# Performance work log

Hardware: AMD Instinct MI355X
Metric: run time of the kernel (lower is better)

## Reference

```python
import jax, jax.numpy as jnp
import numpy as np

N = 50000
E = 400000
IN_DIM = 128
HID = 128
OUT = 128
HEADS = 4
NEG_SLOPE = 0.2
EPS = 1e-16


def setup_inputs() -> dict:
    key = jax.random.key(0)
    ks = jax.random.split(key, 12)
    s = 0.05
    return {
        "x": jax.random.normal(ks[0], (N, IN_DIM), dtype=jnp.float32),
        "edge_index": jax.random.randint(ks[1], (2, E), 0, N, dtype=jnp.int64),
        # layer 1: in_dim -> hid, heads=4, concat
        "W1": jax.random.normal(ks[2], (IN_DIM, HEADS * HID), dtype=jnp.float32) * s,
        "att_src1": jax.random.normal(ks[3], (HEADS, HID), dtype=jnp.float32) * s,
        "att_dst1": jax.random.normal(ks[4], (HEADS, HID), dtype=jnp.float32) * s,
        "bias1": jnp.zeros((HEADS * HID,), dtype=jnp.float32),
        # layer 2: hid*heads -> out, heads=1, no concat
        "W2": jax.random.normal(ks[5], (HEADS * HID, OUT), dtype=jnp.float32) * s,
        "att_src2": jax.random.normal(ks[6], (1, OUT), dtype=jnp.float32) * s,
        "att_dst2": jax.random.normal(ks[7], (1, OUT), dtype=jnp.float32) * s,
        "bias2": jnp.zeros((OUT,), dtype=jnp.float32),
    }


def gat_conv(x, src, dst, W, att_src, att_dst, bias, heads, out_dim, concat):
    n = x.shape[0]
    h = (x @ W).reshape(n, heads, out_dim)                       # [N,H,D]
    a_src = jnp.sum(h * att_src[None], axis=-1)                  # [N,H]
    a_dst = jnp.sum(h * att_dst[None], axis=-1)                  # [N,H]
    e = jax.nn.leaky_relu(a_src[src] + a_dst[dst], NEG_SLOPE)    # [E,H]
    # segment softmax over incoming edges of each dst node
    e_max = jax.ops.segment_max(e, dst, num_segments=n)          # [N,H]
    ex = jnp.exp(e - e_max[dst])
    denom = jax.ops.segment_sum(ex, dst, num_segments=n)         # [N,H]
    alpha = ex / (denom[dst] + EPS)                              # [E,H]
    msg = h[src] * alpha[..., None]                              # [E,H,D]
    out = jax.ops.segment_sum(msg, dst, num_segments=n)          # [N,H,D]
    out = out.reshape(n, heads * out_dim) if concat else out.mean(axis=1)
    return out + bias


def reference(x, edge_index, W1, att_src1, att_dst1, bias1, W2, att_src2, att_dst2, bias2):
    n = x.shape[0]
    loop = jnp.arange(n, dtype=edge_index.dtype)
    src = jnp.concatenate([edge_index[0], loop])  # PyG add_self_loops=True
    dst = jnp.concatenate([edge_index[1], loop])
    h = jax.nn.elu(gat_conv(x, src, dst, W1, att_src1, att_dst1, bias1, HEADS, HID, True))
    z = jax.nn.elu(gat_conv(h, src, dst, W2, att_src2, att_dst2, bias2, 1, OUT, False))
    # F.normalize(z, dim=-1): L2 with eps=1e-12 clamp on the norm
    norm = jnp.maximum(jnp.linalg.norm(z, axis=-1, keepdims=True), 1e-12)
    return z / norm
```

## Files before the change

### kernel.cpp

```cpp
#include <hip/hip_runtime.h>
#include <cstddef>

#define N_NODES 50000
#define N_EDGES 400000
#define TOT_EDGES (N_EDGES + N_NODES)
#define M_PAD 50048
#define SCAN_PAD 50176

typedef _Float16 f16;
typedef __attribute__((ext_vector_type(8))) _Float16 f16x8;
typedef __attribute__((ext_vector_type(4))) _Float16 f16x4;
typedef __attribute__((ext_vector_type(2))) _Float16 f16x2;
typedef __attribute__((ext_vector_type(4))) float f32x4;

__global__ void zero_int(int* __restrict__ p, int n) {
  int i = blockIdx.x * blockDim.x + threadIdx.x;
  if (i < n) p[i] = 0;
}

__global__ void count_kernel(const int* __restrict__ ei, int* __restrict__ cnt) {
  int e = blockIdx.x * blockDim.x + threadIdx.x;
  if (e >= TOT_EDGES) return;
  int dst = (e < N_EDGES) ? ei[N_EDGES + e] : (e - N_EDGES);
  atomicAdd(&cnt[dst], 1);
}

__global__ __launch_bounds__(256) void block_scan(const int* __restrict__ cnt,
                                                  int* __restrict__ pre,
                                                  int* __restrict__ bsum) {
  __shared__ int wsum[4];
  const int t = threadIdx.x, lane = t & 63, w = t >> 6;
  const int base = blockIdx.x * 1024 + t * 4;
  int4 v = *(const int4*)&cnt[base];
  const int s = v.x + v.y + v.z + v.w;
  int x = s;
#pragma unroll
  for (int off = 1; off < 64; off <<= 1) {
    int y = __shfl_up(x, off);
    if (lane >= off) x += y;
  }
  if (lane == 63) wsum[w] = x;
  __syncthreads();
  int woff = 0;
  for (int j = 0; j < w; ++j) woff += wsum[j];
  const int ex = x - s + woff;
  pre[base + 0] = ex;
  pre[base + 1] = ex + v.x;
  pre[base + 2] = ex + v.x + v.y;
  pre[base + 3] = ex + v.x + v.y + v.z;
  if (t == 255) bsum[blockIdx.x] = ex + s;
}

__global__ void bsum_scan(int* __restrict__ bsum, int nb) {
  const int lane = threadIdx.x;
  int v = (lane < nb) ? bsum[lane] : 0;
  int x = v;
#pragma unroll
  for (int off = 1; off < 64; off <<= 1) {
    int y = __shfl_up(x, off);
    if (lane >= off) x += y;
  }
  if (lane < nb) bsum[lane] = x - v;
}

__global__ __launch_bounds__(256) void add_off(int* __restrict__ pre,
                                               const int* __restrict__ boff,
                                               int* __restrict__ cursor) {
  const int base = blockIdx.x * 1024 + threadIdx.x * 4;
  const int off = boff[blockIdx.x];
  int4 v = *(const int4*)&pre[base];
  v.x += off; v.y += off; v.z += off; v.w += off;
  *(int4*)&pre[base] = v;
  *(int4*)&cursor[base] = v;
}

__global__ void fill_kernel(const int* __restrict__ ei, int* __restrict__ cursor,
                            int* __restrict__ csr_src) {
  int e = blockIdx.x * blockDim.x + threadIdx.x;
  if (e >= TOT_EDGES) return;
  int s, d;
  if (e < N_EDGES) { s = ei[e]; d = ei[N_EDGES + e]; }
  else             { s = d = e - N_EDGES; }
  int pos = atomicAdd(&cursor[d], 1);
  csr_src[pos] = s;
}

__global__ __launch_bounds__(256) void prep_x(const float* __restrict__ x,
                                              f16* __restrict__ xb,
                                              const float* __restrict__ V1s,
                                              const float* __restrict__ V1d,
                                              float* __restrict__ as1,
                                              float* __restrict__ ad1) {
  const int wid = (blockIdx.x * 256 + threadIdx.x) >> 6;
  const int lane = threadIdx.x & 63;
  if (wid >= M_PAD) return;
  const int k = lane * 2;
  if (wid >= N_NODES) {
    f16x2 z; z[0] = (f16)0.f; z[1] = (f16)0.f;
    *(f16x2*)&xb[(size_t)wid * 128 + k] = z;
    return;
  }
  float2 xv = *(const float2*)&x[(size_t)wid * 128 + k];
  f16x2 o; o[0] = (f16)xv.x; o[1] = (f16)xv.y;
  *(f16x2*)&xb[(size_t)wid * 128 + k] = o;

  float4 vs0 = *(const float4*)&V1s[k * 4];
  float4 vs1 = *(const float4*)&V1s[(k + 1) * 4];
  float4 vd0 = *(const float4*)&V1d[k * 4];
  float4 vd1 = *(const float4*)&V1d[(k + 1) * 4];
  float s[4], d[4];
  s[0] = xv.x * vs0.x + xv.y * vs1.x;
  s[1] = xv.x * vs0.y + xv.y * vs1.y;
  s[2] = xv.x * vs0.z + xv.y * vs1.z;
  s[3] = xv.x * vs0.w + xv.y * vs1.w;
  d[0] = xv.x * vd0.x + xv.y * vd1.x;
  d[1] = xv.x * vd0.y + xv.y * vd1.y;
  d[2] = xv.x * vd0.z + xv.y * vd1.z;
  d[3] = xv.x * vd0.w + xv.y * vd1.w;
#pragma unroll
  for (int h = 0; h < 4; ++h) {
#pragma unroll
    for (int off = 32; off; off >>= 1) {
      s[h] += __shfl_xor(s[h], off);
      d[h] += __shfl_xor(d[h], off);
    }
  }
  if (lane == 0) {
    *(float4*)&as1[(size_t)wid * 4] = make_float4(s[0], s[1], s[2], s[3]);
    *(float4*)&ad1[(size_t)wid * 4] = make_float4(d[0], d[1], d[2], d[3]);
  }
}

__global__ __launch_bounds__(256) void prep_weights(
    const float* __restrict__ W1, const float* __restrict__ W2,
    const float* __restrict__ att_s1, const float* __restrict__ att_d1,
    const float* __restrict__ att_s2, const float* __restrict__ att_d2,
    f16* __restrict__ w1t, f16* __restrict__ w2t,
    float* __restrict__ V1s, float* __restrict__ V1d,
    float* __restrict__ V2s, float* __restrict__ V2d) {
  const int b = blockIdx.x;
  if (b < 256) {
    const int idx = b * 256 + threadIdx.x;
    const int cc = idx >> 7, rr = idx & 127;
    w1t[idx] = (f16)W1[(size_t)rr * 512 + cc];
  } else if (b < 512) {
    const int idx = (b - 256) * 256 + threadIdx.x;
    const int cc = idx >> 9, rr = idx & 511;
    w2t[idx] = (f16)W2[(size_t)rr * 128 + cc];
  } else if (b < 640) {
    const int wid = (b - 512) * 4 + (threadIdx.x >> 6);
    const int lane = threadIdx.x & 63;
    const int k = wid >> 2, h = wid & 3;
    const float* wrow = W1 + (size_t)k * 512 + h * 128;
    float2 wv = *(const float2*)&wrow[lane * 2];
    float2 sv = *(const float2*)&att_s1[h * 128 + lane * 2];
    float2 dv = *(const float2*)&att_d1[h * 128 + lane * 2];
    float ps = wv.x * sv.x + wv.y * sv.y;
    float pd = wv.x * dv.x + wv.y * dv.y;
#pragma unroll
    for (int off = 32; off; off >>= 1) {
      ps += __shfl_xor(ps, off);
      pd += __shfl_xor(pd, off);
    }
    if (lane == 0) { V1s[k * 4 + h] = ps; V1d[k * 4 + h] = pd; }
  } else {
    const int wid = (b - 640) * 4 + (threadIdx.x >> 6);
    const int lane = threadIdx.x & 63;
    const float* wrow = W2 + (size_t)wid * 128;
    float2 wv = *(const float2*)&wrow[lane * 2];
    float2 sv = *(const float2*)&att_s2[lane * 2];
    float2 dv = *(const float2*)&att_d2[lane * 2];
    float ps = wv.x * sv.x + wv.y * sv.y;
    float pd = wv.x * dv.x + wv.y * dv.y;
#pragma unroll
    for (int off = 32; off; off >>= 1) {
      ps += __shfl_xor(ps, off);
      pd += __shfl_xor(pd, off);
    }
    if (lane == 0) { V2s[wid] = ps; V2d[wid] = pd; }
  }
}

template <int K, bool PER_HEAD>
__global__ __launch_bounds__(256) void gemm_bt(const f16* __restrict__ A, int lda,
                                               const f16* __restrict__ Bt, int ldb,
                                               f16* __restrict__ C, int ldc,
                                               const float* __restrict__ bias) {
  if constexpr (PER_HEAD) {
    const int hh = blockIdx.y;
    A += (size_t)hh * 128;
    Bt += (size_t)hh * 128 * 128;
    C += (size_t)hh * 128;
    bias += hh * 128;
  }
  constexpr int LDT = 40;
  __shared__ __align__(16) f16 As[128 * LDT];
  __shared__ __align__(16) f16 Bs[128 * LDT];
  const int tid = threadIdx.x;
  const int lane = tid & 63;
  const int g = lane >> 4, r16 = lane & 15;
  const int w = tid >> 6, wr = w >> 1, wc = w & 1;
  const long bm = (long)blockIdx.x * 128;

  const int row0 = tid >> 2, h0 = tid & 3;
  const int p1 = (h0 & 1) * 16 + (h0 >> 1) * 4;
  const size_t ga0 = (size_t)(bm + row0) * lda + h0 * 8;
  const size_t ga1 = (size_t)(bm + row0 + 64) * lda + h0 * 8;
  const size_t gb0 = (size_t)row0 * ldb + h0 * 8;
  const size_t gb1 = (size_t)(row0 + 64) * ldb + h0 * 8;
  const int la0 = row0 * LDT + p1, la1 = (row0 + 64) * LDT + p1;

  f32x4 acc[4][4] = {};

  for (int k0 = 0; k0 < K; k0 += 32) {
    __syncthreads();
    f16x8 va0 = *(const f16x8*)&A[ga0 + k0];
    f16x8 va1 = *(const f16x8*)&A[ga1 + k0];
    f16x8 vb0 = *(const f16x8*)&Bt[gb0 + k0];
    f16x8 vb1 = *(const f16x8*)&Bt[gb1 + k0];
    *(f16x4*)&As[la0]     = __builtin_shufflevector(va0, va0, 0, 1, 2, 3);
    *(f16x4*)&As[la0 + 8] = __builtin_shufflevector(va0, va0, 4, 5, 6, 7);
    *(f16x4*)&As[la1]     = __builtin_shufflevector(va1, va1, 0, 1, 2, 3);
    *(f16x4*)&As[la1 + 8] = __builtin_shufflevector(va1, va1, 4, 5, 6, 7);
    *(f16x4*)&Bs[la0]     = __builtin_shufflevector(vb0, vb0, 0, 1, 2, 3);
    *(f16x4*)&Bs[la0 + 8] = __builtin_shufflevector(vb0, vb0, 4, 5, 6, 7);
    *(f16x4*)&Bs[la1]     = __builtin_shufflevector(vb1, vb1, 0, 1, 2, 3);
    *(f16x4*)&Bs[la1 + 8] = __builtin_shufflevector(vb1, vb1, 4, 5, 6, 7);
    __syncthreads();
    f16x8 af[4], bfv[4];
#pragma unroll
    for (int m = 0; m < 4; ++m)
      af[m] = *(const f16x8*)&As[(wr * 64 + m * 16 + r16) * LDT + g * 8];
#pragma unroll
    for (int n = 0; n < 4; ++n)
      bfv[n] = *(const f16x8*)&Bs[(wc * 64 + n * 16 + r16) * LDT + g * 8];
#pragma unroll
    for (int m = 0; m < 4; ++m)
#pragma unroll
      for (int n = 0; n < 4; ++n)
        acc[m][n] = __builtin_amdgcn_mfma_f32_16x16x32_f16(af[m], bfv[n], acc[m][n], 0, 0, 0);
  }

#pragma unroll
  for (int m = 0; m < 4; ++m) {
#pragma unroll
    for (int n = 0; n < 4; ++n) {
      const long row = bm + wr * 64 + m * 16 + g * 4;
      const int col = wc * 64 + n * 16 + r16;
      float bv = 0.f;
      if constexpr (PER_HEAD) bv = bias[col];
#pragma unroll
      for (int r = 0; r < 4; ++r) {
        float v = acc[m][n][r];
        if constexpr (PER_HEAD) {
          v += bv;
          v = v > 0.f ? v : (__expf(v) - 1.f);
        }
        C[(size_t)(row + r) * ldc + col] = (f16)v;
      }
    }
  }
}

__global__ __launch_bounds__(256) void aggregate1x(
    const f16* __restrict__ xsrc, const float* __restrict__ a_src,
    const float* __restrict__ a_dst, const int* __restrict__ rowstart,
    const int* __restrict__ csr, f16* __restrict__ aggb, int n) {
  const int wave = (blockIdx.x * blockDim.x + threadIdx.x) >> 6;
  const int lane = threadIdx.x & 63;
  const int g16 = lane >> 4, l16 = lane & 15;
  const int node = wave * 4 + g16;
  const int col0 = l16 * 8;
  const int rs = rowstart[node];
  const int re = rowstart[node + 1];
  const int deg = re - rs;
  float4 adv = *(const float4*)&a_dst[(size_t)node * 4];

  int maxdeg = deg;
  maxdeg = max(maxdeg, __shfl_xor(maxdeg, 16));
  maxdeg = max(maxdeg, __shfl_xor(maxdeg, 32));

  constexpr int D = 4;
  int sreg[D];
  float4 areg[D];
  f16x8 hreg[D];
#pragma unroll
  for (int p = 0; p < D; ++p) {
    const int k = rs + p;
    const int s = csr[(k < re) ? k : (re - 1)];
    areg[p] = *(const float4*)&a_src[(size_t)s * 4];
    hreg[p] = *(const f16x8*)&xsrc[(size_t)s * 128 + col0];
    const int k2 = rs + D + p;
    sreg[p] = csr[(k2 < re) ? k2 : (re - 1)];
  }

  float acc0[8] = {}, acc1[8] = {}, acc2[8] = {}, acc3[8] = {};
  float Z0 = 0.f, Z1 = 0.f, Z2 = 0.f, Z3 = 0.f;
  for (int base = 0; base < maxdeg; base += D) {
#pragma unroll
    for (int p = 0; p < D; ++p) {
      const int i = base + p;
      const bool act = i < deg;
      float4 av = areg[p];
      float e0 = av.x + adv.x; e0 = e0 > 0.f ? e0 : 0.2f * e0;
      float e1 = av.y + adv.y; e1 = e1 > 0.f ? e1 : 0.2f * e1;
      float e2 = av.z + adv.z; e2 = e2 > 0.f ? e2 : 0.2f * e2;
      float e3 = av.w + adv.w; e3 = e3 > 0.f ? e3 : 0.2f * e3;
      const float w0 = act ? __expf(e0) : 0.f;
      const float w1 = act ? __expf(e1) : 0.f;
      const float w2 = act ? __expf(e2) : 0.f;
      const float w3 = act ? __expf(e3) : 0.f;
      const f16x8 h = hreg[p];
      const int nk = rs + i + D;
      if (nk < re) {
        const int s = sreg[p];
        areg[p] = *(const float4*)&a_src[(size_t)s * 4];
        hreg[p] = *(const f16x8*)&xsrc[(size_t)s * 128 + col0];
      }
      const int nk2 = rs + i + 2 * D;
      if (nk2 < re) sreg[p] = csr[nk2];
      Z0 += w0; Z1 += w1; Z2 += w2; Z3 += w3;
#pragma unroll
      for (int j = 0; j < 8; ++j) {
        const float hv = (float)h[j];
        acc0[j] += w0 * hv;
        acc1[j] += w1 * hv;
        acc2[j] += w2 * hv;
        acc3[j] += w3 * hv;
      }
    }
  }

  const float i0 = 1.f / (Z0 + 1e-16f);
  const float i1 = 1.f / (Z1 + 1e-16f);
  const float i2 = 1.f / (Z2 + 1e-16f);
  const float i3 = 1.f / (Z3 + 1e-16f);
  f16* orow = aggb + (size_t)node * 512 + col0;
  f16x8 o0, o1, o2, o3;
#pragma unroll
  for (int j = 0; j < 8; ++j) {
    o0[j] = (f16)(acc0[j] * i0);
    o1[j] = (f16)(acc1[j] * i1);
    o2[j] = (f16)(acc2[j] * i2);
    o3[j] = (f16)(acc3[j] * i3);
  }
  *(f16x8*)&orow[0]   = o0;
  *(f16x8*)&orow[128] = o1;
  *(f16x8*)&orow[256] = o2;
  *(f16x8*)&orow[384] = o3;
}

__global__ __launch_bounds__(256) void a2_kernel(const f16* __restrict__ h,
                                                 const float* __restrict__ V2s,
                                                 const float* __restrict__ V2d,
                                                 float* __restrict__ as2,
                                                 float* __restrict__ ad2, int n) {
  const int wid = (blockIdx.x * blockDim.x + threadIdx.x) >> 6;
  const int lane = threadIdx.x & 63;
  if (wid >= n) return;
  const int k = lane * 8;
  f16x8 hv = *(const f16x8*)&h[(size_t)wid * 512 + k];
  float4 vsa = *(const float4*)&V2s[k];
  float4 vsb = *(const float4*)&V2s[k + 4];
  float4 vda = *(const float4*)&V2d[k];
  float4 vdb = *(const float4*)&V2d[k + 4];
  float s = (float)hv[0] * vsa.x + (float)hv[1] * vsa.y + (float)hv[2] * vsa.z +
            (float)hv[3] * vsa.w + (float)hv[4] * vsb.x + (float)hv[5] * vsb.y +
            (float)hv[6] * vsb.z + (float)hv[7] * vsb.w;
  float d = (float)hv[0] * vda.x + (float)hv[1] * vda.y + (float)hv[2] * vda.z +
            (float)hv[3] * vda.w + (float)hv[4] * vdb.x + (float)hv[5] * vdb.y +
            (float)hv[6] * vdb.z + (float)hv[7] * vdb.w;
#pragma unroll
  for (int off = 32; off; off >>= 1) {
    s += __shfl_xor(s, off);
    d += __shfl_xor(d, off);
  }
  if (lane == 0) { as2[wid] = s; ad2[wid] = d; }
}

__global__ __launch_bounds__(256) void aggregate2(
    const f16* __restrict__ hsrc, const float* __restrict__ a_src,
    const float* __restrict__ a_dst, const int* __restrict__ rowstart,
    const int* __restrict__ csr, const float* __restrict__ bias,
    float* __restrict__ out, int n) {
  const int wave = (blockIdx.x * blockDim.x + threadIdx.x) >> 6;
  const int lane = threadIdx.x & 63;
  const int g16 = lane >> 4, l16 = lane & 15;
  const int node = wave * 4 + g16;
  const int col0 = l16 * 8;
  const int rs = rowstart[node];
  const int re = rowstart[node + 1];
  const int deg = re - rs;
  const float ad = a_dst[node];

  int maxdeg = deg;
  maxdeg = max(maxdeg, __shfl_xor(maxdeg, 16));
  maxdeg = max(maxdeg, __shfl_xor(maxdeg, 32));

  constexpr int D = 6;
  int sreg[D];
  float areg[D];
  f16x8 hreg[D];
#pragma unroll
  for (int p = 0; p < D; ++p) {
    const int k = rs + p;
    const int s = csr[(k < re) ? k : (re - 1)];
    areg[p] = a_src[s];
    hreg[p] = *(const f16x8*)&hsrc[(size_t)s * 128 + col0];
    const int k2 = rs + D + p;
    sreg[p] = csr[(k2 < re) ? k2 : (re - 1)];
  }

  float acc[8] = {};
  float Z = 0.f;
  for (int base = 0; base < maxdeg; base += D) {
#pragma unroll
    for (int p = 0; p < D; ++p) {
      const int i = base + p;
      const bool act = i < deg;
      float e = areg[p] + ad;
      e = e > 0.f ? e : 0.2f * e;
      const float w = act ? __expf(e) : 0.f;
      const f16x8 h = hreg[p];
      const int nk = rs + i + D;
      if (nk < re) {
        const int s = sreg[p];
        areg[p] = a_src[s];
        hreg[p] = *(const f16x8*)&hsrc[(size_t)s * 128 + col0];
      }
      const int nk2 = rs + i + 2 * D;
      if (nk2 < re) sreg[p] = csr[nk2];
      Z += w;
#pragma unroll
      for (int j = 0; j < 8; ++j) acc[j] += w * (float)h[j];
    }
  }
  const float inv = 1.f / (Z + 1e-16f);

  float4 ba = *(const float4*)&bias[col0];
  float4 bb = *(const float4*)&bias[col0 + 4];
  const float bv[8] = {ba.x, ba.y, ba.z, ba.w, bb.x, bb.y, bb.z, bb.w};
  float v[8];
  float ss = 0.f;
#pragma unroll
  for (int j = 0; j < 8; ++j) {
    float t = acc[j] * inv + bv[j];
    t = t > 0.f ? t : (__expf(t) - 1.f);
    v[j] = t;
    ss += t * t;
  }
  ss += __shfl_xor(ss, 1);
  ss += __shfl_xor(ss, 2);
  ss += __shfl_xor(ss, 4);
  ss += __shfl_xor(ss, 8);
  const float invn = 1.f / fmaxf(sqrtf(ss), 1e-12f);
  float* orow = out + (size_t)node * 128 + col0;
  float4 oa = make_float4(v[0] * invn, v[1] * invn, v[2] * invn, v[3] * invn);
  float4 ob = make_float4(v[4] * invn, v[5] * invn, v[6] * invn, v[7] * invn);
  *(float4*)&orow[0] = oa;
  *(float4*)&orow[4] = ob;
}

extern "C" void kernel_launch(void* const* d_in, const int* in_sizes, int n_in,
                              void* d_out, int out_size, void* d_ws, size_t ws_size,
                              hipStream_t stream) {
  const float* x        = (const float*)d_in[0];
  const int*   ei       = (const int*)d_in[1];
  const float* W1       = (const float*)d_in[2];
  const float* att_src1 = (const float*)d_in[3];
  const float* att_dst1 = (const float*)d_in[4];
  const float* bias1    = (const float*)d_in[5];
  const float* W2       = (const float*)d_in[6];
  const float* att_src2 = (const float*)d_in[7];
  const float* att_dst2 = (const float*)d_in[8];
  const float* bias2    = (const float*)d_in[9];
  float* out = (float*)d_out;

  char* ws = (char*)d_ws;
  size_t off = 0;
  auto alloc = [&](size_t bytes) {
    char* p = ws + off;
    off = (off + bytes + 255) & ~(size_t)255;
    return p;
  };
  f16* xb    = (f16*)alloc(sizeof(f16) * (size_t)M_PAD * 128);
  f16* w1t   = (f16*)alloc(sizeof(f16) * 512 * 128);
  f16* w2t   = (f16*)alloc(sizeof(f16) * 128 * 512);
  f16* aggb  = (f16*)alloc(sizeof(f16) * (size_t)M_PAD * 512);
  f16* out1b = (f16*)alloc(sizeof(f16) * (size_t)M_PAD * 512);
  float* V1s = (float*)alloc(sizeof(float) * 512);
  float* V1d = (float*)alloc(sizeof(float) * 512);
  float* V2s = (float*)alloc(sizeof(float) * 512);
  float* V2d = (float*)alloc(sizeof(float) * 512);
  float* as1 = (float*)alloc(sizeof(float) * N_NODES * 4);
  float* ad1 = (float*)alloc(sizeof(float) * N_NODES * 4);
  float* as2 = (float*)alloc(sizeof(float) * N_NODES);
  float* ad2 = (float*)alloc(sizeof(float) * N_NODES);
  int* rowstart = (int*)alloc(sizeof(int) * (SCAN_PAD + 4));
  int* cursor   = (int*)alloc(sizeof(int) * SCAN_PAD);
  int* bsum     = (int*)alloc(sizeof(int) * 64);
  int* csr      = (int*)alloc(sizeof(int) * TOT_EDGES);
  f16* h2b = aggb;

  const int wgrid  = (N_NODES * 64) / 256;
  const int wgridP = (M_PAD * 64) / 256;

  zero_int<<<(SCAN_PAD + 255) / 256, 256, 0, stream>>>(cursor, SCAN_PAD);
  count_kernel<<<(TOT_EDGES + 255) / 256, 256, 0, stream>>>(ei, cursor);
  block_scan<<<49, 256, 0, stream>>>(cursor, rowstart, bsum);
  bsum_scan<<<1, 64, 0, stream>>>(bsum, 49);
  add_off<<<49, 256, 0, stream>>>(rowstart, bsum, cursor);
  fill_kernel<<<(TOT_EDGES + 255) / 256, 256, 0, stream>>>(ei, cursor, csr);

  prep_weights<<<768, 256, 0, stream>>>(W1, W2, att_src1, att_dst1,
                                        att_src2, att_dst2, w1t, w2t,
                                        V1s, V1d, V2s, V2d);
  prep_x<<<wgridP, 256, 0, stream>>>(x, xb, V1s, V1d, as1, ad1);

  aggregate1x<<<(M_PAD / 4) * 64 / 256, 256, 0, stream>>>(
      xb, as1, ad1, rowstart, csr, aggb, N_NODES);
  gemm_bt<128, true><<<dim3(M_PAD / 128, 4), 256, 0, stream>>>(
      aggb, 512, w1t, 128, out1b, 512, bias1);

  a2_kernel<<<wgrid, 256, 0, stream>>>(out1b, V2s, V2d, as2, ad2, N_NODES);
  gemm_bt<512, false><<<dim3(M_PAD / 128, 1), 256, 0, stream>>>(
      out1b, 512, w2t, 512, h2b, 128, nullptr);
  aggregate2<<<(N_NODES / 4) * 64 / 256, 256, 0, stream>>>(
      h2b, as2, ad2, rowstart, csr, bias2, out, N_NODES);
}
```

Before: 213.2 us.

## Sort nodes by degree for aggregation and fuse layer-2 attention dots into GEMM

Builds a degree histogram and counting-sort order of nodes so each aggregation wave processes four nodes of similar degree, reducing intra-wave divergence from the shared maxdeg loop. The aggregate kernels index nodes through this order, and the padding rows of aggb are now zeroed in prep_x since aggregate1x no longer covers them. The separate a2_kernel pass is removed; its attention projections are computed from the A tiles already loaded inside the layer-2 GEMM. This adds several small launches and atomics for the sort, and aggregation writes become scattered rather than sequential.

```diff
diff --git a/kernel.cpp b/kernel.cpp
--- a/kernel.cpp
+++ b/kernel.cpp
@@ -13,16 +13,23 @@
 typedef __attribute__((ext_vector_type(2))) _Float16 f16x2;
 typedef __attribute__((ext_vector_type(4))) float f32x4;
 
-__global__ void zero_int(int* __restrict__ p, int n) {
-  int i = blockIdx.x * blockDim.x + threadIdx.x;
-  if (i < n) p[i] = 0;
-}
-
-__global__ void count_kernel(const int* __restrict__ ei, int* __restrict__ cnt) {
+__global__ void zero_all(int* __restrict__ deg, int* __restrict__ hist) {
+  int i = blockIdx.x * 256 + threadIdx.x;
+  if (i < SCAN_PAD) deg[i] = 0;
+  else if (i < SCAN_PAD + 128) hist[i - SCAN_PAD] = 0;
+}
+
+__global__ void count_kernel(const int* __restrict__ ei, int* __restrict__ deg) {
   int e = blockIdx.x * blockDim.x + threadIdx.x;
   if (e >= TOT_EDGES) return;
   int dst = (e < N_EDGES) ? ei[N_EDGES + e] : (e - N_EDGES);
-  atomicAdd(&cnt[dst], 1);
+  atomicAdd(&deg[dst], 1);
+}
+
+__global__ void deg_hist(const int* __restrict__ deg, int* __restrict__ hist) {
+  int i = blockIdx.x * 256 + threadIdx.x;
+  if (i >= N_NODES) return;
+  atomicAdd(&hist[min(deg[i], 127)], 1);
 }
 
 __global__ __launch_bounds__(256) void block_scan(const int* __restrict__ cnt,
@@ -51,16 +58,31 @@
   if (t == 255) bsum[blockIdx.x] = ex + s;
 }
 
-__global__ void bsum_scan(int* __restrict__ bsum, int nb) {
-  const int lane = threadIdx.x;
-  int v = (lane < nb) ? bsum[lane] : 0;
-  int x = v;
-#pragma unroll
-  for (int off = 1; off < 64; off <<= 1) {
-    int y = __shfl_up(x, off);
-    if (lane >= off) x += y;
-  }
-  if (lane < nb) bsum[lane] = x - v;
+__global__ void combo_scan(int* __restrict__ bsum, const int* __restrict__ hist,
+                           int* __restrict__ hcur) {
+  const int t = threadIdx.x, lane = t & 63, w = t >> 6;
+  if (w == 0) {
+    int v = (lane < 49) ? bsum[lane] : 0;
+    int x = v;
+#pragma unroll
+    for (int off = 1; off < 64; off <<= 1) {
+      int y = __shfl_up(x, off);
+      if (lane >= off) x += y;
+    }
+    if (lane < 49) bsum[lane] = x - v;
+  } else if (w == 1) {
+    int v0 = hist[lane], v1 = hist[64 + lane];
+    int x0 = v0, x1 = v1;
+#pragma unroll
+    for (int off = 1; off < 64; off <<= 1) {
+      int y0 = __shfl_up(x0, off);
+      int y1 = __shfl_up(x1, off);
+      if (lane >= off) { x0 += y0; x1 += y1; }
+    }
+    const int tot0 = __shfl(x0, 63);
+    hcur[lane] = x0 - v0;
+    hcur[64 + lane] = tot0 + x1 - v1;
+  }
 }
 
 __global__ __launch_bounds__(256) void add_off(int* __restrict__ pre,
@@ -74,6 +96,15 @@
   *(int4*)&cursor[base] = v;
 }
 
+__global__ void scatter_order(const int* __restrict__ deg, int* __restrict__ hcur,
+                              int* __restrict__ order) {
+  int i = blockIdx.x * 256 + threadIdx.x;
+  if (i >= N_NODES) return;
+  const int b = min(deg[i], 127);
+  const int pos = atomicAdd(&hcur[b], 1);
+  order[pos] = i;
+}
+
 __global__ void fill_kernel(const int* __restrict__ ei, int* __restrict__ cursor,
                             int* __restrict__ csr_src) {
   int e = blockIdx.x * blockDim.x + threadIdx.x;
@@ -90,7 +121,8 @@
                                               const float* __restrict__ V1s,
                                               const float* __restrict__ V1d,
                                               float* __restrict__ as1,
-                                              float* __restrict__ ad1) {
+                                              float* __restrict__ ad1,
+                                              f16* __restrict__ aggb) {
   const int wid = (blockIdx.x * 256 + threadIdx.x) >> 6;
   const int lane = threadIdx.x & 63;
   if (wid >= M_PAD) return;
@@ -98,6 +130,10 @@
   if (wid >= N_NODES) {
     f16x2 z; z[0] = (f16)0.f; z[1] = (f16)0.f;
     *(f16x2*)&xb[(size_t)wid * 128 + k] = z;
+    f16x8 z8;
+#pragma unroll
+    for (int j = 0; j < 8; ++j) z8[j] = (f16)0.f;
+    *(f16x8*)&aggb[(size_t)wid * 512 + lane * 8] = z8;
     return;
   }
   float2 xv = *(const float2*)&x[(size_t)wid * 128 + k];
@@ -181,11 +217,15 @@
   }
 }
 
-template <int K, bool PER_HEAD>
+template <int K, bool PER_HEAD, bool FUSE_A2>
 __global__ __launch_bounds__(256) void gemm_bt(const f16* __restrict__ A, int lda,
                                                const f16* __restrict__ Bt, int ldb,
                                                f16* __restrict__ C, int ldc,
-                                               const float* __restrict__ bias) {
+                                               const float* __restrict__ bias,
+                                               const float* __restrict__ V2s,
+                                               const float* __restrict__ V2d,
+                                               float* __restrict__ as2,
+                                               float* __restrict__ ad2) {
   if constexpr (PER_HEAD) {
     const int hh = blockIdx.y;
     A += (size_t)hh * 128;
@@ -211,6 +251,7 @@
   const int la0 = row0 * LDT + p1, la1 = (row0 + 64) * LDT + p1;
 
   f32x4 acc[4][4] = {};
+  float s2a = 0.f, d2a = 0.f, s2b = 0.f, d2b = 0.f;
 
   for (int k0 = 0; k0 < K; k0 += 32) {
     __syncthreads();
@@ -218,6 +259,22 @@
     f16x8 va1 = *(const f16x8*)&A[ga1 + k0];
     f16x8 vb0 = *(const f16x8*)&Bt[gb0 + k0];
     f16x8 vb1 = *(const f16x8*)&Bt[gb1 + k0];
+    if constexpr (FUSE_A2) {
+      const int kc = k0 + h0 * 8;
+      float4 vsa = *(const float4*)&V2s[kc];
+      float4 vsb = *(const float4*)&V2s[kc + 4];
+      float4 vda = *(const float4*)&V2d[kc];
+      float4 vdb = *(const float4*)&V2d[kc + 4];
+      const float vs[8] = {vsa.x, vsa.y, vsa.z, vsa.w, vsb.x, vsb.y, vsb.z, vsb.w};
+      const float vd[8] = {vda.x, vda.y, vda.z, vda.w, vdb.x, vdb.y, vdb.z, vdb.w};
+#pragma unroll
+      for (int j = 0; j < 8; ++j) {
+        s2a += (float)va0[j] * vs[j];
+        d2a += (float)va0[j] * vd[j];
+        s2b += (float)va1[j] * vs[j];
+        d2b += (float)va1[j] * vd[j];
+      }
+    }
     *(f16x4*)&As[la0]     = __builtin_shufflevector(va0, va0, 0, 1, 2, 3);
     *(f16x4*)&As[la0 + 8] = __builtin_shufflevector(va0, va0, 4, 5, 6, 7);
     *(f16x4*)&As[la1]     = __builtin_shufflevector(va1, va1, 0, 1, 2, 3);
@@ -241,6 +298,18 @@
         acc[m][n] = __builtin_amdgcn_mfma_f32_16x16x32_f16(af[m], bfv[n], acc[m][n], 0, 0, 0);
   }
 
+  if constexpr (FUSE_A2) {
+    s2a += __shfl_xor(s2a, 1); s2a += __shfl_xor(s2a, 2);
+    d2a += __shfl_xor(d2a, 1); d2a += __shfl_xor(d2a, 2);
+    s2b += __shfl_xor(s2b, 1); s2b += __shfl_xor(s2b, 2);
+    d2b += __shfl_xor(d2b, 1); d2b += __shfl_xor(d2b, 2);
+    if ((tid & 3) == 0) {
+      const long r0 = bm + row0;
+      as2[r0] = s2a; ad2[r0] = d2a;
+      as2[r0 + 64] = s2b; ad2[r0 + 64] = d2b;
+    }
+  }
+
 #pragma unroll
   for (int m = 0; m < 4; ++m) {
 #pragma unroll
@@ -265,11 +334,12 @@
 __global__ __launch_bounds__(256) void aggregate1x(
     const f16* __restrict__ xsrc, const float* __restrict__ a_src,
     const float* __restrict__ a_dst, const int* __restrict__ rowstart,
-    const int* __restrict__ csr, f16* __restrict__ aggb, int n) {
+    const int* __restrict__ csr, const int* __restrict__ order,
+    f16* __restrict__ aggb) {
   const int wave = (blockIdx.x * blockDim.x + threadIdx.x) >> 6;
   const int lane = threadIdx.x & 63;
   const int g16 = lane >> 4, l16 = lane & 15;
-  const int node = wave * 4 + g16;
+  const int node = order[wave * 4 + g16];
   const int col0 = l16 * 8;
   const int rs = rowstart[node];
   const int re = rowstart[node + 1];
@@ -350,43 +420,15 @@
   *(f16x8*)&orow[384] = o3;
 }
 
-__global__ __launch_bounds__(256) void a2_kernel(const f16* __restrict__ h,
-                                                 const float* __restrict__ V2s,
-                                                 const float* __restrict__ V2d,
-                                                 float* __restrict__ as2,
-                                                 float* __restrict__ ad2, int n) {
-  const int wid = (blockIdx.x * blockDim.x + threadIdx.x) >> 6;
-  const int lane = threadIdx.x & 63;
-  if (wid >= n) return;
-  const int k = lane * 8;
-  f16x8 hv = *(const f16x8*)&h[(size_t)wid * 512 + k];
-  float4 vsa = *(const float4*)&V2s[k];
-  float4 vsb = *(const float4*)&V2s[k + 4];
-  float4 vda = *(const float4*)&V2d[k];
-  float4 vdb = *(const float4*)&V2d[k + 4];
-  float s = (float)hv[0] * vsa.x + (float)hv[1] * vsa.y + (float)hv[2] * vsa.z +
-            (float)hv[3] * vsa.w + (float)hv[4] * vsb.x + (float)hv[5] * vsb.y +
-            (float)hv[6] * vsb.z + (float)hv[7] * vsb.w;
-  float d = (float)hv[0] * vda.x + (float)hv[1] * vda.y + (float)hv[2] * vda.z +
-            (float)hv[3] * vda.w + (float)hv[4] * vdb.x + (float)hv[5] * vdb.y +
-            (float)hv[6] * vdb.z + (float)hv[7] * vdb.w;
-#pragma unroll
-  for (int off = 32; off; off >>= 1) {
-    s += __shfl_xor(s, off);
-    d += __shfl_xor(d, off);
-  }
-  if (lane == 0) { as2[wid] = s; ad2[wid] = d; }
-}
-
 __global__ __launch_bounds__(256) void aggregate2(
     const f16* __restrict__ hsrc, const float* __restrict__ a_src,
     const float* __restrict__ a_dst, const int* __restrict__ rowstart,
-    const int* __restrict__ csr, const float* __restrict__ bias,
-    float* __restrict__ out, int n) {
+    const int* __restrict__ csr, const int* __restrict__ order,
+    const float* __restrict__ bias, float* __restrict__ out) {
   const int wave = (blockIdx.x * blockDim.x + threadIdx.x) >> 6;
   const int lane = threadIdx.x & 63;
   const int g16 = lane >> 4, l16 = lane & 15;
-  const int node = wave * 4 + g16;
+  const int node = order[wave * 4 + g16];
   const int col0 = l16 * 8;
   const int rs = rowstart[node];
   const int re = rowstart[node + 1];
@@ -494,37 +536,40 @@
   float* V2d = (float*)alloc(sizeof(float) * 512);
   float* as1 = (float*)alloc(sizeof(float) * N_NODES * 4);
   float* ad1 = (float*)alloc(sizeof(float) * N_NODES * 4);
-  float* as2 = (float*)alloc(sizeof(float) * N_NODES);
-  float* ad2 = (float*)alloc(sizeof(float) * N_NODES);
+  float* as2 = (float*)alloc(sizeof(float) * M_PAD);
+  float* ad2 = (float*)alloc(sizeof(float) * M_PAD);
   int* rowstart = (int*)alloc(sizeof(int) * (SCAN_PAD + 4));
+  int* deg      = (int*)alloc(sizeof(int) * SCAN_PAD);
   int* cursor   = (int*)alloc(sizeof(int) * SCAN_PAD);
   int* bsum     = (int*)alloc(sizeof(int) * 64);
+  int* hist     = (int*)alloc(sizeof(int) * 128);
+  int* hcur     = (int*)alloc(sizeof(int) * 128);
+  int* order    = (int*)alloc(sizeof(int) * N_NODES);
   int* csr      = (int*)alloc(sizeof(int) * TOT_EDGES);
   f16* h2b = aggb;
 
-  const int wgrid  = (N_NODES * 64) / 256;
   const int wgridP = (M_PAD * 64) / 256;
-
-  zero_int<<<(SCAN_PAD + 255) / 256, 256, 0, stream>>>(cursor, SCAN_PAD);
-  count_kernel<<<(TOT_EDGES + 255) / 256, 256, 0, stream>>>(ei, cursor);
-  block_scan<<<49, 256, 0, stream>>>(cursor, rowstart, bsum);
-  bsum_scan<<<1, 64, 0, stream>>>(bsum, 49);
+  const int agrid  = (N_NODES / 4) * 64 / 256;
+
+  zero_all<<<(SCAN_PAD + 128 + 255) / 256, 256, 0, stream>>>(deg, hist);
+  count_kernel<<<(TOT_EDGES + 255) / 256, 256, 0, stream>>>(ei, deg);
+  deg_hist<<<(N_NODES + 255) / 256, 256, 0, stream>>>(deg, hist);
+  block_scan<<<49, 256, 0, stream>>>(deg, rowstart, bsum);
+  combo_scan<<<1, 256, 0, stream>>>(bsum, hist, hcur);
   add_off<<<49, 256, 0, stream>>>(rowstart, bsum, cursor);
+  scatter_order<<<(N_NODES + 255) / 256, 256, 0, stream>>>(deg, hcur, order);
   fill_kernel<<<(TOT_EDGES + 255) / 256, 256, 0, stream>>>(ei, cursor, csr);
 
   prep_weights<<<768, 256, 0, stream>>>(W1, W2, att_src1, att_dst1,
                                         att_src2, att_dst2, w1t, w2t,
                                         V1s, V1d, V2s, V2d);
-  prep_x<<<wgridP, 256, 0, stream>>>(x, xb, V1s, V1d, as1, ad1);
-
-  aggregate1x<<<(M_PAD / 4) * 64 / 256, 256, 0, stream>>>(
-      xb, as1, ad1, rowstart, csr, aggb, N_NODES);
-  gemm_bt<128, true><<<dim3(M_PAD / 128, 4), 256, 0, stream>>>(
-      aggb, 512, w1t, 128, out1b, 512, bias1);
-
-  a2_kernel<<<wgrid, 256, 0, stream>>>(out1b, V2s, V2d, as2, ad2, N_NODES);
-  gemm_bt<512, false><<<dim3(M_PAD / 128, 1), 256, 0, stream>>>(
-      out1b, 512, w2t, 512, h2b, 128, nullptr);
-  aggregate2<<<(N_NODES / 4) * 64 / 256, 256, 0, stream>>>(
-      h2b, as2, ad2, rowstart, csr, bias2, out, N_NODES);
-}
+  prep_x<<<wgridP, 256, 0, stream>>>(x, xb, V1s, V1d, as1, ad1, aggb);
+
+  aggregate1x<<<agrid, 256, 0, stream>>>(xb, as1, ad1, rowstart, csr, order, aggb);
+  gemm_bt<128, true, false><<<dim3(M_PAD / 128, 4), 256, 0, stream>>>(
+      aggb, 512, w1t, 128, out1b, 512, bias1, nullptr, nullptr, nullptr, nullptr);
+
+  gemm_bt<512, false, true><<<dim3(M_PAD / 128, 1), 256, 0, stream>>>(
+      out1b, 512, w2t, 512, h2b, 128, nullptr, V2s, V2d, as2, ad2);
+  aggregate2<<<agrid, 256, 0, stream>>>(h2b, as2, ad2, rowstart, csr, order, bias2, out);
+}
```

After: 535.7 us. 151% more time.
